# Performance work log

Measured on AMD Instinct MI355X. Metric: run time of the kernel, lower is better.

The kernel has to match this reference:

```python
import jax, jax.numpy as jnp
import numpy as np

NH = 8
DIM = 512
NP = 1024
MNP = 4096
BS = 4
TOPK = 32


def setup_inputs() -> dict:
    key = jax.random.key(0)
    ks = jax.random.split(key, 10)
    q = jax.random.normal(ks[0], (NP, BS, DIM), dtype=jnp.float32)
    k = jax.random.normal(ks[1], (MNP, BS, DIM), dtype=jnp.float32)
    v = jax.random.normal(ks[2], (MNP, BS, DIM), dtype=jnp.float32)
    rns_indices = jax.random.randint(ks[3], (BS, NP, TOPK), 0, MNP)
    s = 0.02
    W1 = jax.random.normal(ks[4], (DIM, DIM), dtype=jnp.float32) * s
    b1 = jnp.zeros((DIM,), dtype=jnp.float32)
    W2 = jax.random.normal(ks[5], (DIM, DIM), dtype=jnp.float32) * s
    b2 = jnp.zeros((DIM,), dtype=jnp.float32)
    W3 = jax.random.normal(ks[6], (DIM, DIM), dtype=jnp.float32) * s
    b3 = jnp.zeros((DIM,), dtype=jnp.float32)
    return {"q": q, "k": k, "v": v, "rns_indices": rns_indices,
            "W1": W1, "b1": b1, "W2": W2, "b2": b2, "W3": W3, "b3": b3}


def reference(q, k, v, rns_indices, W1, b1, W2, b2, W3, b3):
    np_, bs, dim = q.shape
    mnp = k.shape[0]
    nh = NH
    dh = dim // nh
    # seq-first -> batch-first, linear projections (torch Linear: x @ W.T + b)
    qh = (jnp.einsum('nbd,ed->bne', q, W1) + b1).reshape(bs, np_, nh, dh)
    kh = (jnp.einsum('mbd,ed->bme', k, W2) + b2).reshape(bs, mnp, nh, dh)
    vh = (jnp.einsum('mbd,ed->bme', v, W3) + b3).reshape(bs, mnp, nh, dh)
    # dense scores: [bs, nh, np, mnp]
    w = jnp.einsum('bnhd,bmhd->bhnm', qh, kh) / jnp.sqrt(jnp.asarray(dh, w_dtype := qh.dtype))
    # scatter-built neighbor mask: [bs, np, mnp] (shared across heads)
    b_idx = jnp.arange(bs)[:, None, None]
    n_idx = jnp.arange(np_)[None, :, None]
    mask = jnp.zeros((bs, np_, mnp), dtype=w.dtype).at[b_idx, n_idx, rns_indices].set(1.0)
    mask = mask[:, None, :, :]  # broadcast over heads
    w = w * mask + (-1e9) * (1.0 - mask)
    w = jax.nn.softmax(w, axis=3)
    out = jnp.einsum('bhnm,bmhd->nbhd', w, vh).reshape(np_, bs, dim)
    return out
```

## Files before the change

kernel.cpp:

```cpp
#include <hip/hip_runtime.h>
#include <stdint.h>

#define NH   8
#define DIM  512
#define NP   1024
#define MNP  4096
#define BS   4
#define TOPK 32
#define DH   64

typedef unsigned short u16;
typedef __attribute__((ext_vector_type(8))) short bf16x8;
typedef __attribute__((ext_vector_type(4))) float f32x4;

__device__ __forceinline__ u16 f2bf(float f) {
    union { float f; unsigned u; } x; x.f = f;
    unsigned r = x.u + 0x7FFFu + ((x.u >> 16) & 1u);
    return (u16)(r >> 16);
}
__device__ __forceinline__ float bf2f(u16 h) {
    union { unsigned u; float f; } x; x.u = ((unsigned)h) << 16;
    return x.f;
}

__device__ __forceinline__ void async16(const void* g, void* l) {
    __builtin_amdgcn_global_load_lds(
        (const __attribute__((address_space(1))) unsigned int*)g,
        (__attribute__((address_space(3))) unsigned int*)l, 16, 0, 0);
}

__global__ void cvt_all(const float* __restrict__ W1, const float* __restrict__ W2,
                        const float* __restrict__ W3, const float* __restrict__ q,
                        const float* __restrict__ k,  const float* __restrict__ v,
                        u16* __restrict__ wall, u16* __restrict__ act) {
    size_t i = ((size_t)blockIdx.x * 256 + threadIdx.x) * 4;
    const float* s; u16* d;
    if (i < 786432) {
        d = wall + i;
        s = (i < 262144) ? W1 + i : (i < 524288) ? W2 + (i - 262144) : W3 + (i - 524288);
    } else {
        size_t j = i - 786432;
        d = act + j;
        s = (j < 2097152) ? q + j : (j < 10485760) ? k + (j - 2097152) : v + (j - 10485760);
    }
    float4 val = *(const float4*)s;
    ushort4 o;
    o.x = f2bf(val.x); o.y = f2bf(val.y); o.z = f2bf(val.z); o.w = f2bf(val.w);
    *(ushort4*)d = o;
}

__global__ __launch_bounds__(256, 4)
void proj_gemm(const u16* __restrict__ act, const u16* __restrict__ wall,
               const float* __restrict__ b1, const float* __restrict__ b2,
               const float* __restrict__ b3, u16* __restrict__ outall) {
    __shared__ u16 As[128 * 64];
    __shared__ u16 Bs[128 * 64];

    const int z = blockIdx.z;
    if (z == 0 && blockIdx.y >= 32) return;
    const size_t aoff = (z == 0) ? 0u : (z == 1) ? 2097152u : 10485760u;
    const u16* A = act + aoff;
    const u16* W = wall + (size_t)z * 262144;
    const float* bias = (z == 0) ? b1 : (z == 1) ? b2 : b3;
    u16* C = outall + aoff;

    const int tid  = threadIdx.x;
    const int bm   = blockIdx.y * 128;
    const int bn   = blockIdx.x * 128;
    const int wave = tid >> 6;
    const int lane = tid & 63;
    const int wm   = (wave & 1) * 64;
    const int wn   = (wave >> 1) * 64;
    const int l16  = lane & 15;
    const int quad = lane >> 4;

    const int srow = lane >> 3;
    const int scol = ((lane & 7) ^ srow) * 8;

    f32x4 acc[4][4] = {};

    for (int k0 = 0; k0 < 512; k0 += 64) {
        __syncthreads();
#pragma unroll
        for (int r = 0; r < 4; r++) {
            int row = wave * 32 + r * 8;
            async16(A + (size_t)(bm + row + srow) * 512 + k0 + scol,
                    &As[row * 64 + lane * 8]);
            async16(W + (size_t)(bn + row + srow) * 512 + k0 + scol,
                    &Bs[row * 64 + lane * 8]);
        }
        __syncthreads();
#pragma unroll
        for (int kk = 0; kk < 64; kk += 32) {
            bf16x8 af[4], bfr[4];
            const int g = (kk >> 3) + quad;
#pragma unroll
            for (int i = 0; i < 4; i++) {
                int ra = wm + i * 16 + l16;
                int rb = wn + i * 16 + l16;
                af[i]  = *(const bf16x8*)(&As[ra * 64 + ((g ^ (ra & 7)) << 3)]);
                bfr[i] = *(const bf16x8*)(&Bs[rb * 64 + ((g ^ (rb & 7)) << 3)]);
            }
#pragma unroll
            for (int i = 0; i < 4; i++)
#pragma unroll
                for (int j = 0; j < 4; j++)
                    acc[i][j] = __builtin_amdgcn_mfma_f32_16x16x32_bf16(
                        af[i], bfr[j], acc[i][j], 0, 0, 0);
        }
    }
#pragma unroll
    for (int i = 0; i < 4; i++) {
        int row = bm + wm + i * 16 + quad * 4;
#pragma unroll
        for (int j = 0; j < 4; j++) {
            int col = bn + wn + j * 16 + l16;
            float bv = bias[col];
#pragma unroll
            for (int r = 0; r < 4; r++)
                C[(size_t)(row + r) * 512 + col] = f2bf(acc[i][j][r] + bv);
        }
    }
}

__global__ __launch_bounds__(256)
void attn_kernel(const u16* __restrict__ Qh, const u16* __restrict__ Kh,
                 const u16* __restrict__ Vh, const int* __restrict__ rns,
                 float* __restrict__ out) {
    __shared__ float sq[4][512];
    __shared__ float swt[4][32 * 9];
    __shared__ int   srw[4][TOPK];

    const int wv   = threadIdx.x >> 6;
    const int lane = threadIdx.x & 63;
    const int pair = blockIdx.x * 4 + wv;
    const int n = pair >> 2;
    const int b = pair & 3;
    const int s   = lane >> 1;
    const int sub = lane & 1;

    int myidx = rns[(b * NP + n) * TOPK + s];
    int myrow = (myidx * BS + b) * DIM;
    if (sub == 0) srw[wv][s] = myrow;

    bool dup = false;
#pragma unroll
    for (int j = 0; j < TOPK; j++) {
        int other = __shfl(myidx, j * 2, 64);
        dup = dup || ((j < s) && (other == myidx));
    }

    {
        const u16* qrow = Qh + (size_t)pair * DIM;
        uint4 qv = *(const uint4*)(qrow + lane * 8);
        float4 f0 = { bf2f((u16)qv.x), bf2f((u16)(qv.x >> 16)),
                      bf2f((u16)qv.y), bf2f((u16)(qv.y >> 16)) };
        float4 f1 = { bf2f((u16)qv.z), bf2f((u16)(qv.z >> 16)),
                      bf2f((u16)qv.w), bf2f((u16)(qv.w >> 16)) };
        *(float4*)(&sq[wv][lane * 8])     = f0;
        *(float4*)(&sq[wv][lane * 8 + 4]) = f1;
    }
    __builtin_amdgcn_wave_barrier();

    const float* qw = sq[wv];
    float sc[NH];
#pragma unroll
    for (int h = 0; h < NH; h++) {
        const u16* kp = Kh + myrow + h * DH + sub * 32;
        const float* qp = qw + h * DH + sub * 32;
        float acc = 0.f;
#pragma unroll
        for (int d = 0; d < 32; d += 8) {
            uint4 kv = *(const uint4*)(kp + d);
            acc += qp[d + 0] * bf2f((u16)kv.x) + qp[d + 1] * bf2f((u16)(kv.x >> 16))
                 + qp[d + 2] * bf2f((u16)kv.y) + qp[d + 3] * bf2f((u16)(kv.y >> 16))
                 + qp[d + 4] * bf2f((u16)kv.z) + qp[d + 5] * bf2f((u16)(kv.z >> 16))
                 + qp[d + 6] * bf2f((u16)kv.w) + qp[d + 7] * bf2f((u16)(kv.w >> 16));
        }
        sc[h] = acc;
    }
#pragma unroll
    for (int h = 0; h < NH; h++) {
        sc[h] += __shfl_xor(sc[h], 1, 64);
        sc[h] = dup ? -1e30f : sc[h] * 0.125f;
    }
    float w[NH];
#pragma unroll
    for (int h = 0; h < NH; h++) {
        float m = sc[h];
        m = fmaxf(m, __shfl_xor(m, 2, 64));
        m = fmaxf(m, __shfl_xor(m, 4, 64));
        m = fmaxf(m, __shfl_xor(m, 8, 64));
        m = fmaxf(m, __shfl_xor(m, 16, 64));
        m = fmaxf(m, __shfl_xor(m, 32, 64));
        float e = __expf(sc[h] - m);
        float t = e;
        t += __shfl_xor(t, 2, 64);
        t += __shfl_xor(t, 4, 64);
        t += __shfl_xor(t, 8, 64);
        t += __shfl_xor(t, 16, 64);
        t += __shfl_xor(t, 32, 64);
        w[h] = e / t;
    }
    if (sub == 0) {
#pragma unroll
        for (int h = 0; h < NH; h++) swt[wv][s * 9 + h] = w[h];
    }
    __builtin_amdgcn_wave_barrier();

    const int h  = lane >> 3;
    const int e8 = lane * 8;
    float a[8] = {0, 0, 0, 0, 0, 0, 0, 0};
#pragma unroll 8
    for (int si = 0; si < TOPK; si++) {
        int   row = srw[wv][si];
        float wgt = swt[wv][si * 9 + h];
        uint4 vv = *(const uint4*)(Vh + row + e8);
        a[0] += wgt * bf2f((u16)vv.x); a[1] += wgt * bf2f((u16)(vv.x >> 16));
        a[2] += wgt * bf2f((u16)vv.y); a[3] += wgt * bf2f((u16)(vv.y >> 16));
        a[4] += wgt * bf2f((u16)vv.z); a[5] += wgt * bf2f((u16)(vv.z >> 16));
        a[6] += wgt * bf2f((u16)vv.w); a[7] += wgt * bf2f((u16)(vv.w >> 16));
    }
    float* op = out + (size_t)pair * DIM + e8;
    float4 o0 = {a[0], a[1], a[2], a[3]};
    float4 o1 = {a[4], a[5], a[6], a[7]};
    *(float4*)op       = o0;
    *((float4*)op + 1) = o1;
}

extern "C" void kernel_launch(void* const* d_in, const int* in_sizes, int n_in,
                              void* d_out, int out_size, void* d_ws, size_t ws_size,
                              hipStream_t stream) {
    const float* q  = (const float*)d_in[0];
    const float* k  = (const float*)d_in[1];
    const float* v  = (const float*)d_in[2];
    const int* rns  = (const int*)d_in[3];
    const float* W1 = (const float*)d_in[4];
    const float* b1 = (const float*)d_in[5];
    const float* W2 = (const float*)d_in[6];
    const float* b2 = (const float*)d_in[7];
    const float* W3 = (const float*)d_in[8];
    const float* b3 = (const float*)d_in[9];
    float* out = (float*)d_out;

    u16* ws   = (u16*)d_ws;
    u16* wall = ws;
    u16* act  = wall + 786432;
    u16* proj = act + 18874368;
    u16* Qh = proj;
    u16* Kh = proj + 2097152;
    u16* Vh = proj + 10485760;

    cvt_all<<<19200, 256, 0, stream>>>(W1, W2, W3, q, k, v, wall, act);
    proj_gemm<<<dim3(4, 128, 3), 256, 0, stream>>>(act, wall, b1, b2, b3, proj);
    attn_kernel<<<NP * BS / 4, 256, 0, stream>>>(Qh, Kh, Vh, rns, out);
}
```

Measured before the change: 187.7 us.

## Fuse fp32-to-bf16 activation conversion into projection GEMM tile loads

```diff
diff --git a/kernel.cpp b/kernel.cpp
--- a/kernel.cpp
+++ b/kernel.cpp
@@ -22,6 +22,9 @@
     union { unsigned u; float f; } x; x.u = ((unsigned)h) << 16;
     return x.f;
 }
+__device__ __forceinline__ unsigned pack2(float a, float b) {
+    return (unsigned)f2bf(a) | ((unsigned)f2bf(b) << 16);
+}
 
 __device__ __forceinline__ void async16(const void* g, void* l) {
     __builtin_amdgcn_global_load_lds(
@@ -29,44 +32,42 @@
         (__attribute__((address_space(3))) unsigned int*)l, 16, 0, 0);
 }
 
-__global__ void cvt_all(const float* __restrict__ W1, const float* __restrict__ W2,
-                        const float* __restrict__ W3, const float* __restrict__ q,
-                        const float* __restrict__ k,  const float* __restrict__ v,
-                        u16* __restrict__ wall, u16* __restrict__ act) {
-    size_t i = ((size_t)blockIdx.x * 256 + threadIdx.x) * 4;
-    const float* s; u16* d;
-    if (i < 786432) {
-        d = wall + i;
-        s = (i < 262144) ? W1 + i : (i < 524288) ? W2 + (i - 262144) : W3 + (i - 524288);
-    } else {
-        size_t j = i - 786432;
-        d = act + j;
-        s = (j < 2097152) ? q + j : (j < 10485760) ? k + (j - 2097152) : v + (j - 10485760);
-    }
+__global__ void cvt_w(const float* __restrict__ W1, const float* __restrict__ W2,
+                      const float* __restrict__ W3, u16* __restrict__ wall) {
+    int i = (blockIdx.x * 256 + threadIdx.x) * 4;
+    const float* s = (i < 262144) ? W1 + i : (i < 524288) ? W2 + (i - 262144)
+                                           : W3 + (i - 524288);
     float4 val = *(const float4*)s;
     ushort4 o;
     o.x = f2bf(val.x); o.y = f2bf(val.y); o.z = f2bf(val.z); o.w = f2bf(val.w);
-    *(ushort4*)d = o;
+    *(ushort4*)(wall + i) = o;
 }
 
 __global__ __launch_bounds__(256, 4)
-void proj_gemm(const u16* __restrict__ act, const u16* __restrict__ wall,
+void proj_gemm(const float* __restrict__ q, const float* __restrict__ k,
+               const float* __restrict__ v, const u16* __restrict__ wall,
                const float* __restrict__ b1, const float* __restrict__ b2,
                const float* __restrict__ b3, u16* __restrict__ outall) {
     __shared__ u16 As[128 * 64];
     __shared__ u16 Bs[128 * 64];
 
-    const int z = blockIdx.z;
-    if (z == 0 && blockIdx.y >= 32) return;
-    const size_t aoff = (z == 0) ? 0u : (z == 1) ? 2097152u : 10485760u;
-    const u16* A = act + aoff;
+    const int bid = blockIdx.x;
+    const int x = bid & 3;
+    const int t = bid >> 2;
+    int z, y;
+    if (t < 32)       { z = 0; y = t; }
+    else if (t < 160) { z = 1; y = t - 32; }
+    else              { z = 2; y = t - 160; }
+
+    const float* A32 = (z == 0) ? q : (z == 1) ? k : v;
     const u16* W = wall + (size_t)z * 262144;
     const float* bias = (z == 0) ? b1 : (z == 1) ? b2 : b3;
-    u16* C = outall + aoff;
+    const size_t coff = (z == 0) ? 0u : (z == 1) ? 2097152u : 10485760u;
+    u16* C = outall + coff;
 
     const int tid  = threadIdx.x;
-    const int bm   = blockIdx.y * 128;
-    const int bn   = blockIdx.x * 128;
+    const int bm   = y * 128;
+    const int bn   = x * 128;
     const int wave = tid >> 6;
     const int lane = tid & 63;
     const int wm   = (wave & 1) * 64;
@@ -77,17 +78,31 @@
     const int srow = lane >> 3;
     const int scol = ((lane & 7) ^ srow) * 8;
 
+    const int ar = tid >> 1;
+    const int ah = tid & 1;
+
     f32x4 acc[4][4] = {};
 
     for (int k0 = 0; k0 < 512; k0 += 64) {
         __syncthreads();
+        const float* ap = A32 + (size_t)(bm + ar) * 512 + k0 + ah * 32;
+        float4 f[8];
+#pragma unroll
+        for (int i = 0; i < 8; i++) f[i] = *(const float4*)(ap + i * 4);
 #pragma unroll
         for (int r = 0; r < 4; r++) {
             int row = wave * 32 + r * 8;
-            async16(A + (size_t)(bm + row + srow) * 512 + k0 + scol,
-                    &As[row * 64 + lane * 8]);
             async16(W + (size_t)(bn + row + srow) * 512 + k0 + scol,
                     &Bs[row * 64 + lane * 8]);
+        }
+#pragma unroll
+        for (int j = 0; j < 4; j++) {
+            uint4 u;
+            u.x = pack2(f[2 * j].x, f[2 * j].y);
+            u.y = pack2(f[2 * j].z, f[2 * j].w);
+            u.z = pack2(f[2 * j + 1].x, f[2 * j + 1].y);
+            u.w = pack2(f[2 * j + 1].z, f[2 * j + 1].w);
+            *(uint4*)(&As[ar * 64 + (((ah * 4 + j) ^ (ar & 7)) << 3)]) = u;
         }
         __syncthreads();
 #pragma unroll
@@ -245,13 +260,12 @@
 
     u16* ws   = (u16*)d_ws;
     u16* wall = ws;
-    u16* act  = wall + 786432;
-    u16* proj = act + 18874368;
+    u16* proj = wall + 786432;
     u16* Qh = proj;
     u16* Kh = proj + 2097152;
     u16* Vh = proj + 10485760;
 
-    cvt_all<<<19200, 256, 0, stream>>>(W1, W2, W3, q, k, v, wall, act);
-    proj_gemm<<<dim3(4, 128, 3), 256, 0, stream>>>(act, wall, b1, b2, b3, proj);
+    cvt_w<<<768, 256, 0, stream>>>(W1, W2, W3, wall);
+    proj_gemm<<<1152, 256, 0, stream>>>(q, k, v, wall, b1, b2, b3, proj);
     attn_kernel<<<NP * BS / 4, 256, 0, stream>>>(Qh, Kh, Vh, rns, out);
 }
```

Result: slower. 292.5 us (+55.8%).
